# Kernel tuning notes

Measured on AMD Instinct MI355X. Metric: run time of the kernel, lower is better.

The kernel has to match this reference:

```python
import jax, jax.numpy as jnp
import numpy as np

S, B, H, E, V, L = 256, 32, 2000, 512, 10000, 6
EPS = 1e-5

def bn(x, g, b, m, v):
    # eval-mode batch norm over last (feature) dim
    return g * (x - m) * jax.lax.rsqrt(v + EPS) + b

def indrnn(x, u):
    # x: [S, B, F], u: [F]; h_t = relu(x_t + u * h_{t-1})
    def step(h, xt):
        h = jax.nn.relu(xt + u * h)
        return h, h
    h0 = jnp.zeros(x.shape[1:], x.dtype)
    _, ys = jax.lax.scan(step, h0, x)
    return ys

def setup_inputs():
    key = jax.random.key(0)
    ks = jax.random.split(key, 16)
    inp = {}
    inp['tokens'] = jax.random.randint(ks[0], (S, B), 0, V)
    inp['emb'] = jax.random.uniform(ks[1], (V, E), jnp.float32, -0.01, 0.01)
    inp['W0'] = jax.random.normal(ks[2], (E, H), jnp.float32) * (1.0 / np.sqrt(E))
    inp['b0'] = jnp.zeros((H,), jnp.float32)
    inp['Wr'] = jax.random.normal(ks[3], (L - 1, H, H), jnp.float32) * (1.0 / np.sqrt(H))
    inp['br'] = jnp.zeros((L - 1, H), jnp.float32)
    inp['u'] = jax.random.uniform(ks[4], (L, H), jnp.float32, 0.0, 1.0)
    inp['g'] = jnp.ones((L, H), jnp.float32)
    inp['be'] = jnp.zeros((L, H), jnp.float32)
    inp['mu'] = jnp.zeros((L, H), jnp.float32)
    inp['var'] = jnp.ones((L, H), jnp.float32)
    inp['Wl'] = jax.random.normal(ks[5], (H, E), jnp.float32) * (1.0 / np.sqrt(H))
    inp['bl'] = jnp.zeros((E,), jnp.float32)
    inp['ul'] = jax.random.uniform(ks[6], (E,), jnp.float32, 0.0, 1.0)
    inp['gl'] = jnp.ones((E,), jnp.float32)
    inp['bel'] = jnp.zeros((E,), jnp.float32)
    inp['mul'] = jnp.zeros((E,), jnp.float32)
    inp['varl'] = jnp.ones((E,), jnp.float32)
    inp['g2'] = jnp.ones((E,), jnp.float32)
    inp['be2'] = jnp.zeros((E,), jnp.float32)
    inp['mu2'] = jnp.zeros((E,), jnp.float32)
    inp['var2'] = jnp.ones((E,), jnp.float32)
    inp['Wd'] = jax.random.uniform(ks[7], (E, V), jnp.float32, -0.01, 0.01)
    inp['bd'] = jnp.zeros((V,), jnp.float32)
    return inp

def reference(tokens, emb, W0, b0, Wr, br, u, g, be, mu, var,
              Wl, bl, ul, gl, bel, mul, varl, g2, be2, mu2, var2, Wd, bd):
    x = emb[tokens]  # [S, B, E]
    # dropout layers are identity in eval mode
    for l in range(L):
        if l == 0:
            x = jnp.einsum('sbe,eh->sbh', x, W0) + b0
        else:
            x = jnp.einsum('sbh,hk->sbk', x, Wr[l - 1]) + br[l - 1]
        x = bn(x, g[l], be[l], mu[l], var[l])   # bn_before
        x = indrnn(x, u[l])
    x = jnp.einsum('sbh,he->sbe', x, Wl) + bl   # last_fc
    x = bn(x, gl, bel, mul, varl)
    x = indrnn(x, ul)                            # last_indrnn
    x = bn(x, g2, be2, mu2, var2)                # extra_bn (bn_before mode)
    out = (jnp.einsum('sbe,ev->sbv', x, Wd) + bd).reshape(S * B, V)
    return out
```

## Files before the change

### kernel.cpp

```cpp
#include <hip/hip_runtime.h>
#include <hip/hip_bf16.h>

#define S_LEN  256
#define BATCH  32
#define SB     8192
#define EDIM   512
#define HDIM   2000
#define HP     2048
#define VDIM   10000
#define VP     10240
#define EPS_BN 1e-5f

typedef __attribute__((ext_vector_type(8))) short bfx8;
typedef __attribute__((ext_vector_type(4))) float f32x4;

__device__ __forceinline__ void gload_lds16(const void* g, void* l) {
  __builtin_amdgcn_global_load_lds(
      (const __attribute__((address_space(1))) void*)g,
      (__attribute__((address_space(3))) void*)l, 16, 0, 0);
}

__device__ __forceinline__ float bf_lo(unsigned int w) {
  return __builtin_bit_cast(float, (unsigned int)(w << 16));
}
__device__ __forceinline__ float bf_hi(unsigned int w) {
  return __builtin_bit_cast(float, (unsigned int)(w & 0xFFFF0000u));
}
__device__ __forceinline__ unsigned int bf_pack(float lo, float hi) {
  unsigned short a = __builtin_bit_cast(unsigned short, __float2bfloat16(lo));
  unsigned short b = __builtin_bit_cast(unsigned short, __float2bfloat16(hi));
  return (unsigned int)a | ((unsigned int)b << 16);
}

__global__ void transpose_bf16_kernel(const float* __restrict__ W,
                                      __hip_bfloat16* __restrict__ Wt,
                                      int K, int N, int Kp, int Np,
                                      size_t wstride, size_t wtstride) {
  const float* Wb = W + wstride * blockIdx.z;
  __hip_bfloat16* Wtb = Wt + wtstride * blockIdx.z;
  __shared__ float tile[32][33];
  const int tx = threadIdx.x, ty = threadIdx.y;
  const int kb = blockIdx.x * 32, nb = blockIdx.y * 32;
#pragma unroll
  for (int i = 0; i < 4; i++) {
    int k = kb + ty + i * 8, n = nb + tx;
    tile[ty + i * 8][tx] = (k < K && n < N) ? Wb[(size_t)k * N + n] : 0.f;
  }
  __syncthreads();
#pragma unroll
  for (int i = 0; i < 4; i++) {
    int n = nb + ty + i * 8, k = kb + tx;
    if (n < Np && k < Kp) Wtb[(size_t)n * Kp + k] = __float2bfloat16(tile[tx][ty + i * 8]);
  }
}

__global__ void ep_params_kernel(const float* __restrict__ b0, const float* __restrict__ br,
                                 const float* __restrict__ g,  const float* __restrict__ be,
                                 const float* __restrict__ mu, const float* __restrict__ var,
                                 const float* __restrict__ bl, const float* __restrict__ gl,
                                 const float* __restrict__ bel,const float* __restrict__ mul_,
                                 const float* __restrict__ varl,
                                 const float* __restrict__ g2, const float* __restrict__ be2,
                                 const float* __restrict__ mu2,const float* __restrict__ var2,
                                 const float* __restrict__ bd,
                                 float* es, float* eh, float* fs, float* fh,
                                 float* s2, float* h2, float* ds, float* dh) {
  int t = blockIdx.x * 256 + threadIdx.x;
  if (t < 6 * HP) {
    int l = t >> 11, h = t & (HP - 1);
    float sc = 0.f, sh = 0.f;
    if (h < HDIM) {
      float s = g[l * HDIM + h] * rsqrtf(var[l * HDIM + h] + EPS_BN);
      float bias = (l == 0) ? b0[h] : br[(l - 1) * HDIM + h];
      sc = s;
      sh = (bias - mu[l * HDIM + h]) * s + be[l * HDIM + h];
    }
    es[t] = sc; eh[t] = sh;
    return;
  }
  t -= 6 * HP;
  if (t < EDIM) {
    float s = gl[t] * rsqrtf(varl[t] + EPS_BN);
    fs[t] = s; fh[t] = (bl[t] - mul_[t]) * s + bel[t];
    return;
  }
  t -= EDIM;
  if (t < EDIM) {
    float s = g2[t] * rsqrtf(var2[t] + EPS_BN);
    s2[t] = s; h2[t] = be2[t] - mu2[t] * s;
    return;
  }
  t -= EDIM;
  if (t < VP) {
    ds[t] = 1.f; dh[t] = (t < VDIM) ? bd[t] : 0.f;
  }
}

__global__ void gather_emb_kernel(const int* __restrict__ tokens,
                                  const float* __restrict__ emb,
                                  __hip_bfloat16* __restrict__ xb) {
  int idx = blockIdx.x * 256 + threadIdx.x;
  int sb = idx >> 6;
  int e0 = (idx & 63) << 3;
  int tok = tokens[sb];
  const float* src = emb + (size_t)tok * EDIM + e0;
  float4 v0 = ((const float4*)src)[0];
  float4 v1 = ((const float4*)src)[1];
  __hip_bfloat16 tmp[8];
  tmp[0] = __float2bfloat16(v0.x); tmp[1] = __float2bfloat16(v0.y);
  tmp[2] = __float2bfloat16(v0.z); tmp[3] = __float2bfloat16(v0.w);
  tmp[4] = __float2bfloat16(v1.x); tmp[5] = __float2bfloat16(v1.y);
  tmp[6] = __float2bfloat16(v1.z); tmp[7] = __float2bfloat16(v1.w);
  *(bfx8*)&xb[(size_t)sb * EDIM + e0] = *(const bfx8*)tmp;
}

#define BARX  __builtin_amdgcn_s_barrier()
#define SP1   __builtin_amdgcn_s_setprio(1)
#define SP0   __builtin_amdgcn_s_setprio(0)
#define LGKM0 do { asm volatile("s_waitcnt lgkmcnt(0)" ::: "memory"); \
                   __builtin_amdgcn_sched_barrier(0); } while (0)
#define VMC(n) asm volatile("s_waitcnt vmcnt(" #n ")" ::: "memory")

__global__ __launch_bounds__(512, 2) void gemm256p_bf16_kernel(
    const __hip_bfloat16* __restrict__ A, int lda,
    const __hip_bfloat16* __restrict__ Bt, int ldb,
    __hip_bfloat16* __restrict__ Cb, float* __restrict__ Cf, int ldc,
    const float* __restrict__ epS, const float* __restrict__ epH,
    int Kp, int Nstore, int grid_m) {
  __shared__ __align__(16) char smem[131072];
  const int t = threadIdx.x, lane = t & 63, wid = t >> 6;
  const int nwg = gridDim.x, q = nwg >> 3, wg = blockIdx.x;
  const int swzb = (wg & 7) * q + (wg >> 3);
  const int bm = swzb % grid_m, bn = swzb / grid_m;
  const int m0 = bm * 256, n0 = bn * 256;
  const int wm = wid >> 2, wn = wid & 3;

  const int lrow = lane >> 3;
  const int lch  = ((lane & 7) ^ lrow) * 8;
  const __hip_bfloat16* gA = A  + (size_t)(m0 + wid * 8 + lrow) * lda + lch;
  const __hip_bfloat16* gB = Bt + (size_t)(n0 + (wid >> 2) * 64 + (wid & 3) * 8 + lrow) * ldb + lch;
  char* const ldsA = (char*)smem;
  char* const ldsB = (char*)smem + 65536;
  const int laoff = wid * 1024;
  const int lboff = (wid >> 2) * 8192 + (wid & 3) * 1024;

#define STA(buf, e, kt) do {                                                   \
    gload_lds16(gA + (size_t)((e) * 64) * lda + (kt) * 64,                     \
                ldsA + (buf) * 32768 + (e) * 8192 + laoff);                    \
    gload_lds16(gA + (size_t)(128 + (e) * 64) * lda + (kt) * 64,               \
                ldsA + (buf) * 32768 + 16384 + (e) * 8192 + laoff);            \
  } while (0)
#define STB(buf, o, kt) do {                                                   \
    gload_lds16(gB + (size_t)((o) * 32) * ldb + (kt) * 64,                     \
                ldsB + (buf) * 32768 + (o) * 4096 + lboff);                    \
    gload_lds16(gB + (size_t)(128 + (o) * 32) * ldb + (kt) * 64,               \
                ldsB + (buf) * 32768 + 16384 + (o) * 4096 + lboff);            \
  } while (0)

  const int fr = lane & 15, cc = lane >> 4;
  const int sz = (fr & 7) << 4;
  const int ak0 = (cc * 16) ^ sz;
  const int ak1 = (64 + cc * 16) ^ sz;
  const char* rA = (char*)smem + (wm * 128 + fr) * 128;
  const char* rB = (char*)smem + 65536 + (wn * 64 + fr) * 128;

#define RDA(dst, buf, qa) do {                                                 \
    _Pragma("unroll") for (int mi = 0; mi < 4; mi++) {                         \
      dst[mi][0] = *(const bfx8*)(rA + (buf) * 32768 + (qa) * 8192 + mi * 2048 + ak0); \
      dst[mi][1] = *(const bfx8*)(rA + (buf) * 32768 + (qa) * 8192 + mi * 2048 + ak1); \
    } } while (0)
#define RDB(dst, buf, qb) do {                                                 \
    _Pragma("unroll") for (int nf = 0; nf < 2; nf++) {                         \
      dst[nf][0] = *(const bfx8*)(rB + (buf) * 32768 + (qb) * 4096 + nf * 2048 + ak0); \
      dst[nf][1] = *(const bfx8*)(rB + (buf) * 32768 + (qb) * 4096 + nf * 2048 + ak1); \
    } } while (0)
#define MM(qa, qb, aa, bb) do {                                                \
    _Pragma("unroll") for (int mi = 0; mi < 4; mi++)                           \
    _Pragma("unroll") for (int nf = 0; nf < 2; nf++)                           \
    _Pragma("unroll") for (int kk = 0; kk < 2; kk++)                           \
      acc[(qa) * 4 + mi][(qb) * 2 + nf] = __builtin_amdgcn_mfma_f32_16x16x32_bf16( \
          aa[mi][kk], bb[nf][kk], acc[(qa) * 4 + mi][(qb) * 2 + nf], 0, 0, 0); \
  } while (0)

  f32x4 acc[8][4];
#pragma unroll
  for (int i = 0; i < 8; i++)
#pragma unroll
    for (int j = 0; j < 4; j++) acc[i][j] = (f32x4){0.f, 0.f, 0.f, 0.f};

  const int NT = Kp >> 6;
  const int NI = NT >> 1;

  STA(0, 0, 0); STB(0, 0, 0); STB(0, 1, 0); STA(0, 1, 0);
  STA(1, 0, 1); STB(1, 0, 1);
  VMC(4); BARX;

  bfx8 a[4][2], b0[2][2], b2[2][2];
  for (int it = 0; it < NI - 1; ++it) {
    const int kt1 = 2 * it + 1, t2 = 2 * it + 2, t3 = 2 * it + 3;
    RDA(a, 0, 0); RDB(b0, 0, 0); STB(1, 1, kt1);
    BARX; LGKM0; SP1; MM(0, 0, a, b0); SP0; BARX;
    RDB(b2, 0, 1); STA(1, 1, kt1);
    BARX; LGKM0; SP1; MM(0, 1, a, b2); SP0; VMC(6); BARX;
    RDA(a, 0, 1); STA(0, 0, t2);
    BARX; LGKM0; SP1; MM(1, 0, a, b0); SP0; BARX;
    STB(0, 0, t2);
    BARX; LGKM0; SP1; MM(1, 1, a, b2); SP0; VMC(6); BARX;
    RDA(a, 1, 0); RDB(b0, 1, 0); STB(0, 1, t2);
    BARX; LGKM0; SP1; MM(0, 0, a, b0); SP0; BARX;
    RDB(b2, 1, 1); STA(0, 1, t2);
    BARX; LGKM0; SP1; MM(0, 1, a, b2); SP0; VMC(6); BARX;
    RDA(a, 1, 1); STA(1, 0, t3);
    BARX; LGKM0; SP1; MM(1, 0, a, b0); SP0; BARX;
    STB(1, 0, t3);
    BARX; LGKM0; SP1; MM(1, 1, a, b2); SP0; VMC(6); BARX;
  }
  {
    const int kt1 = NT - 1;
    RDA(a, 0, 0); RDB(b0, 0, 0); STB(1, 1, kt1);
    BARX; LGKM0; SP1; MM(0, 0, a, b0); SP0; BARX;
    RDB(b2, 0, 1); STA(1, 1, kt1);
    BARX; LGKM0; SP1; MM(0, 1, a, b2); SP0; VMC(6); BARX;
    RDA(a, 0, 1);
    BARX; LGKM0; SP1; MM(1, 0, a, b0); SP0; BARX;
    BARX; LGKM0; SP1; MM(1, 1, a, b2); SP0; VMC(2); BARX;
    RDA(a, 1, 0); RDB(b0, 1, 0);
    BARX; LGKM0; SP1; MM(0, 0, a, b0); SP0; BARX;
    RDB(b2, 1, 1);
    BARX; LGKM0; SP1; MM(0, 1, a, b2); SP0; VMC(0); BARX;
    RDA(a, 1, 1);
    BARX; LGKM0; SP1; MM(1, 0, a, b0); SP0; BARX;
    BARX; LGKM0; SP1; MM(1, 1, a, b2); SP0; BARX;
  }
  VMC(0);

  const int colb = n0 + wn * 64 + fr;
  const int rowb = m0 + wm * 128 + cc * 4;
#pragma unroll
  for (int nf = 0; nf < 4; nf++) {
    int col = colb + nf * 16;
    if (col >= Nstore) continue;
    float sc = epS[col], sh = epH[col];
    if (Cf) {
#pragma unroll
      for (int mf = 0; mf < 8; mf++)
#pragma unroll
        for (int rr = 0; rr < 4; rr++)
          Cf[(size_t)(rowb + mf * 16 + rr) * ldc + col] = acc[mf][nf][rr] * sc + sh;
    } else {
#pragma unroll
      for (int mf = 0; mf < 8; mf++)
#pragma unroll
        for (int rr = 0; rr < 4; rr++)
          Cb[(size_t)(rowb + mf * 16 + rr) * ldc + col] =
              __float2bfloat16(acc[mf][nf][rr] * sc + sh);
    }
  }
}

__global__ __launch_bounds__(256, 2) void gemm128_bf16_kernel(
    const __hip_bfloat16* __restrict__ A, int lda,
    const __hip_bfloat16* __restrict__ Bt, int ldb,
    __hip_bfloat16* __restrict__ C, int ldc,
    const float* __restrict__ epS, const float* __restrict__ epH,
    int Kp, int Nstore) {
  __shared__ __align__(16) __hip_bfloat16 As[128 * 32];
  __shared__ __align__(16) __hip_bfloat16 Bs[128 * 32];
  const int t = threadIdx.x;
  const int lane = t & 63;
  const int wave = t >> 6;
  const int m0 = blockIdx.x * 128;
  const int n0 = blockIdx.y * 128;
  const int wm = (wave >> 1) * 64;
  const int wn = (wave & 1) * 64;

  f32x4 acc[4][4];
#pragma unroll
  for (int i = 0; i < 4; i++)
#pragma unroll
    for (int j = 0; j < 4; j++) acc[i][j] = (f32x4){0.f, 0.f, 0.f, 0.f};

  const int kc = (t & 3) * 8;
  for (int k0 = 0; k0 < Kp; k0 += 32) {
#pragma unroll
    for (int r = 0; r < 2; r++) {
      int row = (r * 256 + t) >> 2;
      gload_lds16(A  + (size_t)(m0 + row) * lda + k0 + kc, &As[(r * 256 + (wave << 6)) * 8]);
      gload_lds16(Bt + (size_t)(n0 + row) * ldb + k0 + kc, &Bs[(r * 256 + (wave << 6)) * 8]);
    }
    __syncthreads();

    bfx8 af[4], bfr[4];
    const int fr = lane & 15;
    const int ko = (lane >> 4) * 8;
#pragma unroll
    for (int f = 0; f < 4; f++) af[f]  = *(const bfx8*)&As[(wm + f * 16 + fr) * 32 + ko];
#pragma unroll
    for (int f = 0; f < 4; f++) bfr[f] = *(const bfx8*)&Bs[(wn + f * 16 + fr) * 32 + ko];
#pragma unroll
    for (int i = 0; i < 4; i++)
#pragma unroll
      for (int j = 0; j < 4; j++)
        acc[i][j] = __builtin_amdgcn_mfma_f32_16x16x32_bf16(af[i], bfr[j], acc[i][j], 0, 0, 0);
    __syncthreads();
  }

  const int colb = n0 + wn + (lane & 15);
  const int rowb = m0 + wm + ((lane >> 4) << 2);
#pragma unroll
  for (int j = 0; j < 4; j++) {
    int col = colb + j * 16;
    if (col >= Nstore) continue;
    float sc = epS[col], sh = epH[col];
#pragma unroll
    for (int i = 0; i < 4; i++)
#pragma unroll
      for (int r = 0; r < 4; r++)
        C[(size_t)(rowb + i * 16 + r) * ldc + col] =
            __float2bfloat16(acc[i][j][r] * sc + sh);
  }
}

__global__ __launch_bounds__(64) void scan_hidden_kernel(
    const __hip_bfloat16* __restrict__ y, const float* __restrict__ u,
    __hip_bfloat16* __restrict__ xb) {
  const int t = blockIdx.x * 64 + threadIdx.x;
  const int h0 = (t & (HP / 2 - 1)) * 2;
  float u0 = 0.f, u1 = 0.f;
  if (h0 < HDIM) { u0 = u[h0]; u1 = (h0 + 1 < HDIM) ? u[h0 + 1] : 0.f; }
  const unsigned int* yp = (const unsigned int*)y;
  unsigned int* xp = (unsigned int*)xb;
  const size_t stride = BATCH * HP / 2;
  float hv0 = 0.f, hv1 = 0.f;
  unsigned int q0[8], q1[8], q2[8], q3[8];
#define LD8(Q, bi) do { size_t o = (size_t)t + (size_t)(bi) * 8 * stride;       \
    _Pragma("unroll") for (int j = 0; j < 8; j++) Q[j] = yp[o + (size_t)j * stride]; \
  } while (0)
#define PR8(Q, bi) do { size_t o = (size_t)t + (size_t)(bi) * 8 * stride;       \
    _Pragma("unroll") for (int j = 0; j < 8; j++) {                             \
      hv0 = fmaxf(fmaf(u0, hv0, bf_lo(Q[j])), 0.f);                             \
      hv1 = fmaxf(fmaf(u1, hv1, bf_hi(Q[j])), 0.f);                             \
      xp[o + (size_t)j * stride] = bf_pack(hv0, hv1); }                         \
  } while (0)
  LD8(q0, 0); LD8(q1, 1); LD8(q2, 2);
  for (int c = 0; c < 32; c += 4) {
    LD8(q3, c + 3);
    PR8(q0, c);
    if (c + 4 < 32) LD8(q0, c + 4);
    PR8(q1, c + 1);
    if (c + 5 < 32) LD8(q1, c + 5);
    PR8(q2, c + 2);
    if (c + 6 < 32) LD8(q2, c + 6);
    PR8(q3, c + 3);
  }
#undef LD8
#undef PR8
}

__global__ __launch_bounds__(64) void scan_final_kernel(
    const __hip_bfloat16* __restrict__ y, const float* __restrict__ ul,
    const float* __restrict__ s2, const float* __restrict__ h2,
    __hip_bfloat16* __restrict__ xb) {
  const int t = blockIdx.x * 64 + threadIdx.x;
  const int e0 = (t & (EDIM / 2 - 1)) * 2;
  const float u0 = ul[e0], u1 = ul[e0 + 1];
  const float sc0 = s2[e0], sh0 = h2[e0], sc1 = s2[e0 + 1], sh1 = h2[e0 + 1];
  const unsigned int* yp = (const unsigned int*)y;
  unsigned int* xp = (unsigned int*)xb;
  const size_t stride = BATCH * EDIM / 2;
  float hv0 = 0.f, hv1 = 0.f;
  unsigned int q0[8], q1[8], q2[8], q3[8];
#define LD8(Q, bi) do { size_t o = (size_t)t + (size_t)(bi) * 8 * stride;       \
    _Pragma("unroll") for (int j = 0; j < 8; j++) Q[j] = yp[o + (size_t)j * stride]; \
  } while (0)
#define PR8(Q, bi) do { size_t o = (size_t)t + (size_t)(bi) * 8 * stride;       \
    _Pragma("unroll") for (int j = 0; j < 8; j++) {                             \
      hv0 = fmaxf(fmaf(u0, hv0, bf_lo(Q[j])), 0.f);                             \
      hv1 = fmaxf(fmaf(u1, hv1, bf_hi(Q[j])), 0.f);                             \
      xp[o + (size_t)j * stride] = bf_pack(hv0 * sc0 + sh0, hv1 * sc1 + sh1); } \
  } while (0)
  LD8(q0, 0); LD8(q1, 1); LD8(q2, 2);
  for (int c = 0; c < 32; c += 4) {
    LD8(q3, c + 3);
    PR8(q0, c);
    if (c + 4 < 32) LD8(q0, c + 4);
    PR8(q1, c + 1);
    if (c + 5 < 32) LD8(q1, c + 5);
    PR8(q2, c + 2);
    if (c + 6 < 32) LD8(q2, c + 6);
    PR8(q3, c + 3);
  }
#undef LD8
#undef PR8
}

extern "C" void kernel_launch(void* const* d_in, const int* in_sizes, int n_in,
                              void* d_out, int out_size, void* d_ws, size_t ws_size,
                              hipStream_t stream) {
  const int*   tokens = (const int*)d_in[0];
  const float* emb  = (const float*)d_in[1];
  const float* W0   = (const float*)d_in[2];
  const float* b0   = (const float*)d_in[3];
  const float* Wr   = (const float*)d_in[4];
  const float* br   = (const float*)d_in[5];
  const float* u    = (const float*)d_in[6];
  const float* g    = (const float*)d_in[7];
  const float* be   = (const float*)d_in[8];
  const float* mu   = (const float*)d_in[9];
  const float* var  = (const float*)d_in[10];
  const float* Wl   = (const float*)d_in[11];
  const float* bl   = (const float*)d_in[12];
  const float* ul   = (const float*)d_in[13];
  const float* gl   = (const float*)d_in[14];
  const float* bel  = (const float*)d_in[15];
  const float* mul_ = (const float*)d_in[16];
  const float* varl = (const float*)d_in[17];
  const float* g2   = (const float*)d_in[18];
  const float* be2  = (const float*)d_in[19];
  const float* mu2  = (const float*)d_in[20];
  const float* var2 = (const float*)d_in[21];
  const float* Wd   = (const float*)d_in[22];
  const float* bd   = (const float*)d_in[23];
  float* out = (float*)d_out;

  char* w = (char*)d_ws;
  auto carve = [&](size_t bytes) { void* p = (void*)w; w += (bytes + 255) & ~(size_t)255; return p; };
  __hip_bfloat16* wt0 = (__hip_bfloat16*)carve((size_t)HP * EDIM * 2);
  __hip_bfloat16* wtr = (__hip_bfloat16*)carve((size_t)5 * HP * HP * 2);
  __hip_bfloat16* wtl = (__hip_bfloat16*)carve((size_t)EDIM * HP * 2);
  __hip_bfloat16* wtd = (__hip_bfloat16*)carve((size_t)VP * EDIM * 2);
  __hip_bfloat16* xb  = (__hip_bfloat16*)carve((size_t)SB * HP * 2);
  __hip_bfloat16* yb  = (__hip_bfloat16*)carve((size_t)SB * HP * 2);
  float* es  = (float*)carve((size_t)6 * HP * 4);
  float* eh  = (float*)carve((size_t)6 * HP * 4);
  float* fs  = (float*)carve((size_t)EDIM * 4);
  float* fh  = (float*)carve((size_t)EDIM * 4);
  float* s2b = (float*)carve((size_t)EDIM * 4);
  float* h2b = (float*)carve((size_t)EDIM * 4);
  float* dsb = (float*)carve((size_t)VP * 4);
  float* dhb = (float*)carve((size_t)VP * 4);

  dim3 tb32(32, 8);
  transpose_bf16_kernel<<<dim3(EDIM / 32, HP / 32, 1), tb32, 0, stream>>>(
      W0, wt0, EDIM, HDIM, EDIM, HP, 0, 0);
  transpose_bf16_kernel<<<dim3(HP / 32, HP / 32, 5), tb32, 0, stream>>>(
      Wr, wtr, HDIM, HDIM, HP, HP, (size_t)HDIM * HDIM, (size_t)HP * HP);
  transpose_bf16_kernel<<<dim3(HP / 32, EDIM / 32, 1), tb32, 0, stream>>>(
      Wl, wtl, HDIM, EDIM, HP, EDIM, 0, 0);
  transpose_bf16_kernel<<<dim3(EDIM / 32, VP / 32, 1), tb32, 0, stream>>>(
      Wd, wtd, EDIM, VDIM, EDIM, VP, 0, 0);

  ep_params_kernel<<<(6 * HP + 2 * EDIM + VP) / 256, 256, 0, stream>>>(
      b0, br, g, be, mu, var, bl, gl, bel, mul_, varl, g2, be2, mu2, var2, bd,
      es, eh, fs, fh, s2b, h2b, dsb, dhb);

  gather_emb_kernel<<<SB * EDIM / 8 / 256, 256, 0, stream>>>(tokens, emb, xb);

  gemm256p_bf16_kernel<<<(SB / 256) * (HP / 256), 512, 0, stream>>>(
      xb, EDIM, wt0, EDIM, yb, nullptr, HP, es, eh, EDIM, HP, SB / 256);
  scan_hidden_kernel<<<BATCH * HP / 2 / 64, 64, 0, stream>>>(yb, u, xb);

  for (int l = 1; l < 6; l++) {
    gemm256p_bf16_kernel<<<(SB / 256) * (HP / 256), 512, 0, stream>>>(
        xb, HP, wtr + (size_t)(l - 1) * HP * HP, HP, yb, nullptr, HP,
        es + l * HP, eh + l * HP, HP, HP, SB / 256);
    scan_hidden_kernel<<<BATCH * HP / 2 / 64, 64, 0, stream>>>(yb, u + (size_t)l * HDIM, xb);
  }

  gemm128_bf16_kernel<<<dim3(SB / 128, EDIM / 128), 256, 0, stream>>>(
      xb, HP, wtl, HP, yb, EDIM, fs, fh, HP, EDIM);
  scan_final_kernel<<<BATCH * EDIM / 2 / 64, 64, 0, stream>>>(yb, ul, s2b, h2b, xb);

  gemm256p_bf16_kernel<<<(SB / 256) * (VP / 256), 512, 0, stream>>>(
      xb, EDIM, wtd, EDIM, nullptr, out, VDIM, dsb, dhb, EDIM, VDIM, SB / 256);
}
```

Baseline: 733.4 us.

## Fuse IndRNN scan into GEMM epilogue via batch-major row layout

Reorders activations from (s,b) row order to (b,s) order so each 256-row GEMM tile holds the full sequence for one batch element. The hidden-layer GEMM epilogue then stages the tile in LDS and runs the recurrent scan per column, which removes the separate scan kernels and one full read and write of the intermediate activations per layer. The final scan and output GEMM are adapted to the new ordering, and the output rows are scattered back to the original order. In exchange, the serial 256-step scan now runs on only half the threads of each GEMM block, and its global stores are strided by row.

```diff
diff --git a/kernel.cpp b/kernel.cpp
--- a/kernel.cpp
+++ b/kernel.cpp
@@ -10,6 +10,7 @@
 #define VDIM   10000
 #define VP     10240
 #define EPS_BN 1e-5f
+
 
 typedef __attribute__((ext_vector_type(8))) short bfx8;
 typedef __attribute__((ext_vector_type(4))) float f32x4;
@@ -100,9 +101,10 @@
                                   const float* __restrict__ emb,
                                   __hip_bfloat16* __restrict__ xb) {
   int idx = blockIdx.x * 256 + threadIdx.x;
-  int sb = idx >> 6;
+  int mprime = idx >> 6;
   int e0 = (idx & 63) << 3;
-  int tok = tokens[sb];
+  int s = mprime & 255, b = mprime >> 8;
+  int tok = tokens[s * BATCH + b];
   const float* src = emb + (size_t)tok * EDIM + e0;
   float4 v0 = ((const float4*)src)[0];
   float4 v1 = ((const float4*)src)[1];
@@ -111,7 +113,7 @@
   tmp[2] = __float2bfloat16(v0.z); tmp[3] = __float2bfloat16(v0.w);
   tmp[4] = __float2bfloat16(v1.x); tmp[5] = __float2bfloat16(v1.y);
   tmp[6] = __float2bfloat16(v1.z); tmp[7] = __float2bfloat16(v1.w);
-  *(bfx8*)&xb[(size_t)sb * EDIM + e0] = *(const bfx8*)tmp;
+  *(bfx8*)&xb[(size_t)mprime * EDIM + e0] = *(const bfx8*)tmp;
 }
 
 #define BARX  __builtin_amdgcn_s_barrier()
@@ -126,6 +128,7 @@
     const __hip_bfloat16* __restrict__ Bt, int ldb,
     __hip_bfloat16* __restrict__ Cb, float* __restrict__ Cf, int ldc,
     const float* __restrict__ epS, const float* __restrict__ epH,
+    const float* __restrict__ uscan,
     int Kp, int Nstore, int grid_m) {
   __shared__ __align__(16) char smem[131072];
   const int t = threadIdx.x, lane = t & 63, wid = t >> 6;
@@ -235,7 +238,50 @@
   VMC(0);
 
   const int colb = n0 + wn * 64 + fr;
-  const int rowb = m0 + wm * 128 + cc * 4;
+  const int rowb = wm * 128 + cc * 4;
+
+  if (uscan) {
+    unsigned short* lds16 = (unsigned short*)smem;
+    const int colL0 = wn * 64 + fr;
+#pragma unroll
+    for (int nf = 0; nf < 4; nf++) {
+      int colL = colL0 + nf * 16;
+      float sc = epS[n0 + colL], sh = epH[n0 + colL];
+#pragma unroll
+      for (int mf = 0; mf < 8; mf++) {
+#pragma unroll
+        for (int rr = 0; rr < 4; rr++) {
+          int s = rowb + mf * 16 + rr;
+          int byte = ((s << 9) + (colL << 1)) ^ (((s >> 2) & 3) << 5);
+          lds16[byte >> 1] = __builtin_bit_cast(unsigned short,
+              __float2bfloat16(acc[mf][nf][rr] * sc + sh));
+        }
+      }
+    }
+    __syncthreads();
+    if (t < 256) {
+      const int c = t;
+      const float uu = (n0 + c < HDIM) ? uscan[n0 + c] : 0.f;
+      float h = 0.f;
+      __hip_bfloat16* xcol = Cb + (size_t)m0 * ldc + n0 + c;
+      for (int s8 = 0; s8 < 256; s8 += 8) {
+        unsigned short vv[8];
+#pragma unroll
+        for (int j = 0; j < 8; j++) {
+          int s = s8 + j;
+          int byte = ((s << 9) + (c << 1)) ^ (((s >> 2) & 3) << 5);
+          vv[j] = lds16[byte >> 1];
+        }
+#pragma unroll
+        for (int j = 0; j < 8; j++) {
+          h = fmaxf(fmaf(uu, h, bf_lo((unsigned int)vv[j])), 0.f);
+          xcol[(size_t)(s8 + j) * ldc] = __float2bfloat16(h);
+        }
+      }
+    }
+    return;
+  }
+
 #pragma unroll
   for (int nf = 0; nf < 4; nf++) {
     int col = colb + nf * 16;
@@ -245,14 +291,16 @@
 #pragma unroll
       for (int mf = 0; mf < 8; mf++)
 #pragma unroll
+        for (int rr = 0; rr < 4; rr++) {
+          int s = rowb + mf * 16 + rr;
+          Cf[(size_t)(s * BATCH + bm) * ldc + col] = acc[mf][nf][rr] * sc + sh;
+        }
+    } else {
+#pragma unroll
+      for (int mf = 0; mf < 8; mf++)
+#pragma unroll
         for (int rr = 0; rr < 4; rr++)
-          Cf[(size_t)(rowb + mf * 16 + rr) * ldc + col] = acc[mf][nf][rr] * sc + sh;
-    } else {
-#pragma unroll
-      for (int mf = 0; mf < 8; mf++)
-#pragma unroll
-        for (int rr = 0; rr < 4; rr++)
-          Cb[(size_t)(rowb + mf * 16 + rr) * ldc + col] =
+          Cb[(size_t)(m0 + rowb + mf * 16 + rr) * ldc + col] =
               __float2bfloat16(acc[mf][nf][rr] * sc + sh);
     }
   }
@@ -321,59 +369,26 @@
   }
 }
 
-__global__ __launch_bounds__(64) void scan_hidden_kernel(
-    const __hip_bfloat16* __restrict__ y, const float* __restrict__ u,
-    __hip_bfloat16* __restrict__ xb) {
-  const int t = blockIdx.x * 64 + threadIdx.x;
-  const int h0 = (t & (HP / 2 - 1)) * 2;
-  float u0 = 0.f, u1 = 0.f;
-  if (h0 < HDIM) { u0 = u[h0]; u1 = (h0 + 1 < HDIM) ? u[h0 + 1] : 0.f; }
-  const unsigned int* yp = (const unsigned int*)y;
-  unsigned int* xp = (unsigned int*)xb;
-  const size_t stride = BATCH * HP / 2;
-  float hv0 = 0.f, hv1 = 0.f;
-  unsigned int q0[8], q1[8], q2[8], q3[8];
-#define LD8(Q, bi) do { size_t o = (size_t)t + (size_t)(bi) * 8 * stride;       \
-    _Pragma("unroll") for (int j = 0; j < 8; j++) Q[j] = yp[o + (size_t)j * stride]; \
-  } while (0)
-#define PR8(Q, bi) do { size_t o = (size_t)t + (size_t)(bi) * 8 * stride;       \
-    _Pragma("unroll") for (int j = 0; j < 8; j++) {                             \
-      hv0 = fmaxf(fmaf(u0, hv0, bf_lo(Q[j])), 0.f);                             \
-      hv1 = fmaxf(fmaf(u1, hv1, bf_hi(Q[j])), 0.f);                             \
-      xp[o + (size_t)j * stride] = bf_pack(hv0, hv1); }                         \
-  } while (0)
-  LD8(q0, 0); LD8(q1, 1); LD8(q2, 2);
-  for (int c = 0; c < 32; c += 4) {
-    LD8(q3, c + 3);
-    PR8(q0, c);
-    if (c + 4 < 32) LD8(q0, c + 4);
-    PR8(q1, c + 1);
-    if (c + 5 < 32) LD8(q1, c + 5);
-    PR8(q2, c + 2);
-    if (c + 6 < 32) LD8(q2, c + 6);
-    PR8(q3, c + 3);
-  }
-#undef LD8
-#undef PR8
-}
-
 __global__ __launch_bounds__(64) void scan_final_kernel(
     const __hip_bfloat16* __restrict__ y, const float* __restrict__ ul,
     const float* __restrict__ s2, const float* __restrict__ h2,
     __hip_bfloat16* __restrict__ xb) {
   const int t = blockIdx.x * 64 + threadIdx.x;
-  const int e0 = (t & (EDIM / 2 - 1)) * 2;
+  const int e2 = t & (EDIM / 2 - 1);
+  const int b  = t >> 8;
+  const int e0 = e2 * 2;
   const float u0 = ul[e0], u1 = ul[e0 + 1];
   const float sc0 = s2[e0], sh0 = h2[e0], sc1 = s2[e0 + 1], sh1 = h2[e0 + 1];
   const unsigned int* yp = (const unsigned int*)y;
   unsigned int* xp = (unsigned int*)xb;
-  const size_t stride = BATCH * EDIM / 2;
+  const size_t base0 = (size_t)b * 256 * (EDIM / 2) + e2;
+  const size_t stride = EDIM / 2;
   float hv0 = 0.f, hv1 = 0.f;
   unsigned int q0[8], q1[8], q2[8], q3[8];
-#define LD8(Q, bi) do { size_t o = (size_t)t + (size_t)(bi) * 8 * stride;       \
+#define LD8(Q, bi) do { size_t o = base0 + (size_t)(bi) * 8 * stride;           \
     _Pragma("unroll") for (int j = 0; j < 8; j++) Q[j] = yp[o + (size_t)j * stride]; \
   } while (0)
-#define PR8(Q, bi) do { size_t o = (size_t)t + (size_t)(bi) * 8 * stride;       \
+#define PR8(Q, bi) do { size_t o = base0 + (size_t)(bi) * 8 * stride;           \
     _Pragma("unroll") for (int j = 0; j < 8; j++) {                             \
       hv0 = fmaxf(fmaf(u0, hv0, bf_lo(Q[j])), 0.f);                             \
       hv1 = fmaxf(fmaf(u1, hv1, bf_hi(Q[j])), 0.f);                             \
@@ -430,7 +445,8 @@
   __hip_bfloat16* wtl = (__hip_bfloat16*)carve((size_t)EDIM * HP * 2);
   __hip_bfloat16* wtd = (__hip_bfloat16*)carve((size_t)VP * EDIM * 2);
   __hip_bfloat16* xb  = (__hip_bfloat16*)carve((size_t)SB * HP * 2);
-  __hip_bfloat16* yb  = (__hip_bfloat16*)carve((size_t)SB * HP * 2);
+  __hip_bfloat16* xb2 = (__hip_bfloat16*)carve((size_t)SB * HP * 2);
+  __hip_bfloat16* yb  = (__hip_bfloat16*)carve((size_t)SB * EDIM * 2);
   float* es  = (float*)carve((size_t)6 * HP * 4);
   float* eh  = (float*)carve((size_t)6 * HP * 4);
   float* fs  = (float*)carve((size_t)EDIM * 4);
@@ -456,21 +472,22 @@
 
   gather_emb_kernel<<<SB * EDIM / 8 / 256, 256, 0, stream>>>(tokens, emb, xb);
 
+  __hip_bfloat16* src = xb;
+  __hip_bfloat16* dst = xb2;
   gemm256p_bf16_kernel<<<(SB / 256) * (HP / 256), 512, 0, stream>>>(
-      xb, EDIM, wt0, EDIM, yb, nullptr, HP, es, eh, EDIM, HP, SB / 256);
-  scan_hidden_kernel<<<BATCH * HP / 2 / 64, 64, 0, stream>>>(yb, u, xb);
-
+      src, EDIM, wt0, EDIM, dst, nullptr, HP, es, eh, u, EDIM, HP, SB / 256);
+  { __hip_bfloat16* tmp = src; src = dst; dst = tmp; }
   for (int l = 1; l < 6; l++) {
     gemm256p_bf16_kernel<<<(SB / 256) * (HP / 256), 512, 0, stream>>>(
-        xb, HP, wtr + (size_t)(l - 1) * HP * HP, HP, yb, nullptr, HP,
-        es + l * HP, eh + l * HP, HP, HP, SB / 256);
-    scan_hidden_kernel<<<BATCH * HP / 2 / 64, 64, 0, stream>>>(yb, u + (size_t)l * HDIM, xb);
+        src, HP, wtr + (size_t)(l - 1) * HP * HP, HP, dst, nullptr, HP,
+        es + l * HP, eh + l * HP, u + (size_t)l * HDIM, HP, HP, SB / 256);
+    __hip_bfloat16* tmp = src; src = dst; dst = tmp;
   }
 
   gemm128_bf16_kernel<<<dim3(SB / 128, EDIM / 128), 256, 0, stream>>>(
-      xb, HP, wtl, HP, yb, EDIM, fs, fh, HP, EDIM);
-  scan_final_kernel<<<BATCH * EDIM / 2 / 64, 64, 0, stream>>>(yb, ul, s2b, h2b, xb);
+      src, HP, wtl, HP, yb, EDIM, fs, fh, HP, EDIM);
+  scan_final_kernel<<<BATCH * EDIM / 2 / 64, 64, 0, stream>>>(yb, ul, s2b, h2b, dst);
 
   gemm256p_bf16_kernel<<<(SB / 256) * (VP / 256), 512, 0, stream>>>(
-      xb, EDIM, wtd, EDIM, nullptr, out, VDIM, dsb, dhb, EDIM, VDIM, SB / 256);
-}
+      dst, EDIM, wtd, EDIM, nullptr, out, VDIM, dsb, dhb, nullptr, EDIM, VDIM, SB / 256);
+}
```

New measurement: 623.1 us. 1.18x faster.
